# Kernel optimization log

Measured on AMD Instinct MI355X. Metric: run time of the kernel, lower is better.

The kernel has to match this reference:

```python
import jax, jax.numpy as jnp
import numpy as np

EMBED = 512
HEADS = 8
DH = EMBED // HEADS  # 64
M = 256              # num_landmarks
ITERS = 6            # pinv iterations
SCALE = DH ** -0.5
RES_K = 33           # lucidrains residual_conv_kernel default


def _layer_norm(x, g, b, eps=1e-5):
    mu = jnp.mean(x, axis=-1, keepdims=True)
    var = jnp.mean((x - mu) ** 2, axis=-1, keepdims=True)
    return (x - mu) / jnp.sqrt(var + eps) * g + b


def _pinv_iter(x, iters=ITERS):
    # Moore-Penrose iterative pseudo-inverse (lucidrains nystrom-attention)
    abs_x = jnp.abs(x)
    denom = jnp.max(abs_x.sum(-1)) * jnp.max(abs_x.sum(-2))
    z = jnp.swapaxes(x, -1, -2) / denom
    I = jnp.eye(x.shape[-1], dtype=x.dtype)
    for _ in range(iters):
        xz = x @ z
        z = 0.25 * z @ (13 * I - xz @ (15 * I - xz @ (7 * I - xz)))
    return z


def _dwconv2d(x, w, b):
    # x: [B,C,H,W], w: [C,1,kh,kw] depthwise, SAME padding (odd kernels == k//2)
    out = jax.lax.conv_general_dilated(x, w, (1, 1), 'SAME',
                                       dimension_numbers=('NCHW', 'OIHW', 'NCHW'),
                                       feature_group_count=x.shape[1])
    return out + b[None, :, None, None]


def _nystrom_attn(x, Wqkv, Wo, bo, res_w):
    # x: [B, n, EMBED]; pad at FRONT so n divisible by M (matches F.pad(..., padding, 0) semantics)
    b, n, _ = x.shape
    pad = (M - n % M) % M
    x = jnp.pad(x, ((0, 0), (pad, 0), (0, 0)))
    npad = n + pad
    qkv = x @ Wqkv.T                               # [b, npad, 3*EMBED]
    q, k, v = jnp.split(qkv, 3, axis=-1)
    to_heads = lambda t: t.reshape(b, npad, HEADS, DH).transpose(0, 2, 1, 3)  # bhnd
    q, k, v = to_heads(q), to_heads(k), to_heads(v)
    q = q * SCALE
    l = npad // M
    q_land = q.reshape(b, HEADS, M, l, DH).mean(3)  # [b,h,M,d]
    k_land = k.reshape(b, HEADS, M, l, DH).mean(3)
    s1 = jnp.einsum('bhnd,bhmd->bhnm', q, k_land)
    s2 = jnp.einsum('bhmd,bhld->bhml', q_land, k_land)
    s3 = jnp.einsum('bhmd,bhnd->bhmn', q_land, k)
    a1 = jax.nn.softmax(s1, -1)
    a2 = jax.nn.softmax(s2, -1)
    a3 = jax.nn.softmax(s3, -1)
    a2_inv = _pinv_iter(a2)
    out = a1 @ (a2_inv @ (a3 @ v))                 # [b,h,npad,d]
    # residual depthwise conv over v: channels=heads, spatial=(npad, DH), kernel (33,1)
    res = jax.lax.conv_general_dilated(v, res_w, (1, 1), 'SAME',
                                       dimension_numbers=('NCHW', 'OIHW', 'NCHW'),
                                       feature_group_count=HEADS)
    out = out + res
    out = out.transpose(0, 2, 1, 3).reshape(b, npad, EMBED)
    out = out @ Wo.T + bo
    return out[:, -n:]                             # drop front padding


def setup_inputs() -> dict:
    key = jax.random.key(0)
    ks = jax.random.split(key, 32)
    s = 0.02
    inp = {}
    inp['data'] = jax.random.normal(ks[0], (4, 4096, 1536), jnp.float32)
    inp['W1'] = jax.random.normal(ks[1], (EMBED, 1536), jnp.float32) * s
    inp['b1'] = jnp.zeros((EMBED,), jnp.float32)
    inp['cls_token'] = jax.random.normal(ks[2], (1, 1, EMBED), jnp.float32)
    for li, base in ((1, 3), (2, 9)):
        inp[f'ln{li}_g'] = jnp.ones((EMBED,), jnp.float32)
        inp[f'ln{li}_b'] = jnp.zeros((EMBED,), jnp.float32)
        inp[f'Wqkv{li}'] = jax.random.normal(ks[base], (3 * EMBED, EMBED), jnp.float32) * s
        inp[f'Wo{li}'] = jax.random.normal(ks[base + 1], (EMBED, EMBED), jnp.float32) * s
        inp[f'bo{li}'] = jnp.zeros((EMBED,), jnp.float32)
        inp[f'res{li}'] = jax.random.normal(ks[base + 2], (HEADS, 1, RES_K, 1), jnp.float32) * s
    inp['pw7'] = jax.random.normal(ks[15], (EMBED, 1, 7, 7), jnp.float32) * s
    inp['pb7'] = jnp.zeros((EMBED,), jnp.float32)
    inp['pw5'] = jax.random.normal(ks[16], (EMBED, 1, 5, 5), jnp.float32) * s
    inp['pb5'] = jnp.zeros((EMBED,), jnp.float32)
    inp['pw3'] = jax.random.normal(ks[17], (EMBED, 1, 3, 3), jnp.float32) * s
    inp['pb3'] = jnp.zeros((EMBED,), jnp.float32)
    inp['lnf_g'] = jnp.ones((EMBED,), jnp.float32)
    inp['lnf_b'] = jnp.zeros((EMBED,), jnp.float32)
    inp['W2'] = jax.random.normal(ks[18], (2, EMBED), jnp.float32) * s
    inp['b2'] = jnp.zeros((2,), jnp.float32)
    return inp


def reference(data, W1, b1, cls_token, ln1_g, ln1_b, Wqkv1, Wo1, bo1, res1,
              ln2_g, ln2_b, Wqkv2, Wo2, bo2, res2,
              pw7, pb7, pw5, pb5, pw3, pb3, lnf_g, lnf_b, W2, b2):
    h = jax.nn.relu(data @ W1.T + b1)              # [B, N, EMBED]
    B, N, C = h.shape
    grid = int(np.ceil(np.sqrt(N)))
    add = grid * grid - N
    if add > 0:
        h = jnp.concatenate([h, h[:, :add]], axis=1)
    cls = jnp.broadcast_to(cls_token, (B, 1, C))
    h = jnp.concatenate([cls, h], axis=1)          # [B, 1+grid^2, C]
    # TransLayer 1
    h = h + _nystrom_attn(_layer_norm(h, ln1_g, ln1_b), Wqkv1, Wo1, bo1, res1)
    # PPEG
    cls_t, feat = h[:, :1], h[:, 1:]
    cnn = feat.transpose(0, 2, 1).reshape(B, C, grid, grid)
    x = _dwconv2d(cnn, pw7, pb7) + cnn + _dwconv2d(cnn, pw5, pb5) + _dwconv2d(cnn, pw3, pb3)
    feat = x.reshape(B, C, grid * grid).transpose(0, 2, 1)
    h = jnp.concatenate([cls_t, feat], axis=1)
    # TransLayer 2
    h = h + _nystrom_attn(_layer_norm(h, ln2_g, ln2_b), Wqkv2, Wo2, bo2, res2)
    h = _layer_norm(h, lnf_g, lnf_b)
    cls_feat = h[:, 0]
    logits = cls_feat @ W2.T + b2
    Y_prob = jax.nn.softmax(logits, -1)
    Y_hat = jnp.argmax(Y_prob, -1)
    return logits, Y_prob, Y_hat
```

## Files before the change

### kernel.cpp

```cpp
#include <hip/hip_runtime.h>
#include <math.h>

#define EMBED 512
#define HEADS 8
#define DH 64
#define MM 256
#define LSEG 17
#define NPAD 4352
#define NTOK 4097
#define N0 4096
#define BATCH 4
#define CIN 1536
#define QSCALE 0.125f
#define BH 32
#define NSEG 17

typedef float fp32x4 __attribute__((ext_vector_type(4)));
typedef short bf16x8 __attribute__((ext_vector_type(8)));
typedef short bf16x4 __attribute__((ext_vector_type(4)));
typedef unsigned short u16;

__device__ __forceinline__ unsigned short f2bf(float f) {
  unsigned int u = __float_as_uint(f);
  u += 0x7fffu + ((u >> 16) & 1u);
  return (unsigned short)(u >> 16);
}
__device__ __forceinline__ float bf2f(unsigned short u) {
  return __uint_as_float((unsigned)u << 16);
}

__device__ __forceinline__ float block_sum(float v, float* red) {
  #pragma unroll
  for (int o = 1; o < 64; o <<= 1) v += __shfl_xor(v, o);
  int lane = threadIdx.x & 63, wid = threadIdx.x >> 6;
  if (lane == 0) red[wid] = v;
  __syncthreads();
  float r = red[0] + red[1] + red[2] + red[3];
  __syncthreads();
  return r;
}
__device__ __forceinline__ float block_max(float v, float* red) {
  #pragma unroll
  for (int o = 1; o < 64; o <<= 1) v = fmaxf(v, __shfl_xor(v, o));
  int lane = threadIdx.x & 63, wid = threadIdx.x >> 6;
  if (lane == 0) red[wid] = v;
  __syncthreads();
  float r = fmaxf(fmaxf(red[0], red[1]), fmaxf(red[2], red[3]));
  __syncthreads();
  return r;
}

__global__ void f2bf_kernel(const float* __restrict__ in, u16* __restrict__ out, int n) {
  int t = (blockIdx.x * 256 + threadIdx.x) * 8;
  if (t >= n) return;
  float4 a = *(const float4*)&in[t];
  float4 b = *(const float4*)&in[t + 4];
  bf16x8 pk;
  pk[0]=(short)f2bf(a.x); pk[1]=(short)f2bf(a.y); pk[2]=(short)f2bf(a.z); pk[3]=(short)f2bf(a.w);
  pk[4]=(short)f2bf(b.x); pk[5]=(short)f2bf(b.y); pk[6]=(short)f2bf(b.z); pk[7]=(short)f2bf(b.w);
  *(bf16x8*)&out[t] = pk;
}

__global__ __launch_bounds__(256) void gemm_abt(
    const u16* __restrict__ A, const u16* __restrict__ W,
    int Mrows, int Ncols, int K, const float* __restrict__ bias,
    float* __restrict__ fout, float* __restrict__ fout2,
    u16* __restrict__ uo0, u16* __restrict__ uo1, u16* __restrict__ uo2,
    int mode)
{
  __shared__ u16 As[64][40];
  __shared__ u16 Ws[128][40];
  int tid = threadIdx.x;
  int lane = tid & 63;
  int wv = tid >> 6;
  int rowBase = blockIdx.y * 64, colBase = blockIdx.x * 128;
  int quad = lane >> 4;
  int l15 = lane & 15;
  int sr = tid >> 2;
  int skc = (tid & 3) * 8;

  fp32x4 acc[8];
  #pragma unroll
  for (int i = 0; i < 8; i++) acc[i] = fp32x4{0,0,0,0};

  for (int kb = 0; kb < K; kb += 32) {
    __syncthreads();
    {
      int grow = rowBase + sr;
      bf16x8 av;
      if (grow < Mrows) av = *(const bf16x8*)&A[(size_t)grow * K + kb + skc];
      else { bf16x8 z = {0,0,0,0,0,0,0,0}; av = z; }
      *(bf16x8*)&As[sr][skc] = av;
    }
    #pragma unroll
    for (int h = 0; h < 2; h++) {
      int r = sr + h * 64;
      *(bf16x8*)&Ws[r][skc] =
          *(const bf16x8*)&W[(size_t)(colBase + r) * K + kb + skc];
    }
    __syncthreads();
    bf16x8 aF = *(const bf16x8*)&As[wv * 16 + l15][quad * 8];
    #pragma unroll
    for (int ct = 0; ct < 8; ct++) {
      bf16x8 bF = *(const bf16x8*)&Ws[ct * 16 + l15][quad * 8];
      acc[ct] = __builtin_amdgcn_mfma_f32_16x16x32_bf16(aF, bF, acc[ct], 0, 0, 0);
    }
  }

  #pragma unroll
  for (int ct = 0; ct < 8; ct++) {
    int col = colBase + ct * 16 + l15;
    #pragma unroll
    for (int i = 0; i < 4; i++) {
      int row = rowBase + wv * 16 + quad * 4 + i;
      if (row >= Mrows) continue;
      float v = acc[ct][i];
      if (mode == 0) {
        v += bias[col];
        v = fmaxf(v, 0.f);
        int b = row / N0, n = row % N0;
        fout[((size_t)b * NTOK + 1 + n) * EMBED + col] = v;
      } else if (mode == 1) {
        int b = row / NPAD, n = row % NPAD;
        int sec = col / EMBED;
        int hh = (col % EMBED) / DH;
        int d = col & 63;
        u16* dst = (sec == 0) ? uo0 : ((sec == 1) ? uo1 : uo2);
        if (sec == 0) v *= QSCALE;
        dst[(((size_t)b * HEADS + hh) * NPAD + n) * DH + d] = f2bf(v);
      } else if (mode == 2) {
        v += bias[col];
        fout[(size_t)row * EMBED + col] += v;
      } else {
        v += bias[col];
        float full = fout[(size_t)row * EMBED + col] + v;
        fout[(size_t)row * EMBED + col] = full;
        int b = row / NTOK, t = row % NTOK;
        if (t > 0) fout2[((size_t)b * N0 + (t - 1)) * EMBED + col] = full;
      }
    }
  }
}

__global__ __launch_bounds__(256) void gemm_nn2(
    const u16* __restrict__ A, const u16* __restrict__ Bc,
    u16* __restrict__ Cr, u16* __restrict__ Cc,
    int Nsize, float beta, float sgn, float gamma)
{
  __shared__ u16 As[64][40];
  __shared__ u16 Bs[64][40];
  int batch = blockIdx.z;
  const u16* Ab = A + (size_t)batch * MM * MM;
  const u16* Bb = Bc + (size_t)batch * MM * Nsize;
  int tid = threadIdx.x;
  int lane = tid & 63, wv = tid >> 6, quad = lane >> 4, l15 = lane & 15;
  int rowBase = blockIdx.y * 64, colBase = blockIdx.x * 64;
  int sr = tid >> 2, skc = (tid & 3) * 8;
  fp32x4 acc[4] = {fp32x4{0,0,0,0}, fp32x4{0,0,0,0}, fp32x4{0,0,0,0}, fp32x4{0,0,0,0}};

  for (int kb = 0; kb < MM; kb += 32) {
    __syncthreads();
    *(bf16x8*)&As[sr][skc] = *(const bf16x8*)&Ab[(size_t)(rowBase + sr) * MM + kb + skc];
    *(bf16x8*)&Bs[sr][skc] = *(const bf16x8*)&Bb[(size_t)(colBase + sr) * MM + kb + skc];
    __syncthreads();
    bf16x8 aF = *(const bf16x8*)&As[wv * 16 + l15][quad * 8];
    #pragma unroll
    for (int ct = 0; ct < 4; ct++) {
      bf16x8 bF = *(const bf16x8*)&Bs[ct * 16 + l15][quad * 8];
      acc[ct] = __builtin_amdgcn_mfma_f32_16x16x32_bf16(aF, bF, acc[ct], 0, 0, 0);
    }
  }

  #pragma unroll
  for (int ct = 0; ct < 4; ct++) {
    int col = colBase + ct * 16 + l15;
    #pragma unroll
    for (int i = 0; i < 4; i++) {
      int row = rowBase + wv * 16 + quad * 4 + i;
      float v = sgn * acc[ct][i];
      if (beta != 0.f) v += beta * bf2f(Ab[(size_t)row * MM + col]);
      v *= gamma;
      u16 o = f2bf(v);
      if (Cr) Cr[(size_t)batch * MM * Nsize + (size_t)row * Nsize + col] = o;
      if (Cc) Cc[(size_t)batch * MM * Nsize + (size_t)col * MM + row] = o;
    }
  }
}

__global__ void cls_kernel(const float* __restrict__ cls, float* __restrict__ h) {
  int t = blockIdx.x * blockDim.x + threadIdx.x;
  if (t >= BATCH * EMBED) return;
  int b = t / EMBED, c = t % EMBED;
  h[(size_t)b * NTOK * EMBED + c] = cls[c];
}

__global__ void zero_pad_kernel(u16* __restrict__ xpad) {
  int t = blockIdx.x * blockDim.x + threadIdx.x;
  const int per = 255 * EMBED;
  if (t >= BATCH * per) return;
  int b = t / per, r = t % per;
  xpad[(size_t)b * NPAD * EMBED + r] = 0;
}

__global__ __launch_bounds__(256) void ln_pad_kernel(
    const float* __restrict__ h, const float* __restrict__ g,
    const float* __restrict__ be, u16* __restrict__ xpad)
{
  __shared__ float red[4];
  int row = blockIdx.x;
  int b = row / NTOK, j = row % NTOK;
  const float* x = h + (size_t)row * EMBED;
  int tid = threadIdx.x;
  float v0 = x[tid], v1 = x[tid + 256];
  float mu = block_sum(v0 + v1, red) * (1.f / 512.f);
  float d0 = v0 - mu, d1 = v1 - mu;
  float var = block_sum(d0 * d0 + d1 * d1, red) * (1.f / 512.f);
  float inv = 1.f / sqrtf(var + 1e-5f);
  u16* o = xpad + ((size_t)b * NPAD + 255 + j) * EMBED;
  o[tid]       = f2bf(d0 * inv * g[tid]       + be[tid]);
  o[tid + 256] = f2bf(d1 * inv * g[tid + 256] + be[tid + 256]);
}

__global__ __launch_bounds__(256) void landmarks_kernel(
    const u16* __restrict__ q, const u16* __restrict__ k,
    float* __restrict__ qland, float* __restrict__ kland)
{
  int bh = blockIdx.y;
  int m = blockIdx.x * 4 + (threadIdx.x >> 6);
  int d = threadIdx.x & 63;
  const u16* qb = q + (size_t)bh * NPAD * DH;
  const u16* kb = k + (size_t)bh * NPAD * DH;
  float sq = 0.f, sk = 0.f;
  int base = m * LSEG;
  #pragma unroll
  for (int t = 0; t < LSEG; t++) {
    sq += bf2f(qb[(size_t)(base + t) * DH + d]);
    sk += bf2f(kb[(size_t)(base + t) * DH + d]);
  }
  qland[((size_t)bh * MM + m) * DH + d] = sq * (1.f / LSEG);
  kland[((size_t)bh * MM + m) * DH + d] = sk * (1.f / LSEG);
}

__global__ __launch_bounds__(256) void s2_softmax_kernel(
    const float* __restrict__ qland, const float* __restrict__ kland,
    u16* __restrict__ a2)
{
  __shared__ float qrow[64];
  __shared__ float red[4];
  int bh = blockIdx.y, m = blockIdx.x, tid = threadIdx.x;
  if (tid < 64) qrow[tid] = qland[((size_t)bh * MM + m) * DH + tid];
  __syncthreads();
  const float* kb = kland + (size_t)bh * MM * DH + (size_t)tid * DH;
  float s = 0.f;
  #pragma unroll 16
  for (int d = 0; d < 64; d++) s += qrow[d] * kb[d];
  float mx = block_max(s, red);
  float e = __expf(s - mx);
  float tot = block_sum(e, red);
  a2[((size_t)bh * MM + m) * MM + tid] = f2bf(e / tot);
}

__global__ void init_denom_kernel(float* __restrict__ denoms) {
  if (threadIdx.x < 2) denoms[threadIdx.x] = 0.f;
}

__global__ __launch_bounds__(256) void denom_kernel(
    const u16* __restrict__ a2, float* __restrict__ denoms)
{
  __shared__ float red[4];
  int bh = blockIdx.x, tid = threadIdx.x;
  const u16* A = a2 + (size_t)bh * MM * MM;
  float rs = 0.f, cs = 0.f;
  for (int j = 0; j < MM; j++) rs += bf2f(A[(size_t)tid * MM + j]);
  for (int i = 0; i < MM; i++) cs += bf2f(A[(size_t)i * MM + tid]);
  float mr = block_max(rs, red);
  float mc = block_max(cs, red);
  if (tid == 0) {
    atomicMax((int*)&denoms[0], __float_as_int(mr));
    atomicMax((int*)&denoms[1], __float_as_int(mc));
  }
}

__global__ __launch_bounds__(256) void z0_trans_kernel(
    const u16* __restrict__ a2, const float* __restrict__ denoms,
    u16* __restrict__ zr, u16* __restrict__ zc)
{
  __shared__ u16 tile[64][72];
  int bh = blockIdx.z, i0 = blockIdx.y * 64, j0 = blockIdx.x * 64;
  int tid = threadIdx.x;
  float inv = 1.f / (denoms[0] * denoms[1]);
  const u16* Ab = a2 + (size_t)bh * MM * MM;
  #pragma unroll
  for (int it = 0; it < 4; it++) {
    int idx = it * 1024 + tid * 4;
    int r = idx >> 6, c = idx & 63;
    bf16x4 v = *(const bf16x4*)&Ab[(size_t)(i0 + r) * MM + j0 + c];
    u16 o[4];
    #pragma unroll
    for (int j = 0; j < 4; j++) o[j] = f2bf(bf2f((unsigned short)v[j]) * inv);
    *(bf16x4*)&zc[(size_t)bh * MM * MM + (size_t)(i0 + r) * MM + j0 + c] = *(bf16x4*)o;
    #pragma unroll
    for (int j = 0; j < 4; j++) tile[c + j][r] = o[j];
  }
  __syncthreads();
  #pragma unroll
  for (int it = 0; it < 4; it++) {
    int idx = it * 1024 + tid * 4;
    int r = idx >> 6, c = idx & 63;
    u16 o[4] = {tile[r][c], tile[r][c + 1], tile[r][c + 2], tile[r][c + 3]};
    *(bf16x4*)&zr[(size_t)bh * MM * MM + (size_t)(j0 + r) * MM + i0 + c] = *(bf16x4*)o;
  }
}

__global__ __launch_bounds__(256) void a3v_part_mfma(
    const float* __restrict__ qland, const u16* __restrict__ k,
    const u16* __restrict__ v, u16* __restrict__ Opart,
    float* __restrict__ mpart, float* __restrict__ lpart)
{
  __shared__ __align__(16) u16 qs[64][40];
  __shared__ __align__(16) u16 ks[256][72];
  __shared__ __align__(16) u16 vt[64][72];
  int tid = threadIdx.x;
  int lane = tid & 63, wv = tid >> 6, quad = lane >> 4, l15 = lane & 15;
  int bh = blockIdx.y;
  int ltile = blockIdx.x & 3;
  int seg = blockIdx.x >> 2;
  int l0 = ltile * 64;
  int key0 = seg * 256;
  const float* qb = qland + (size_t)bh * MM * DH;
  const u16* kb = k + (size_t)bh * NPAD * DH;
  const u16* vb = v + (size_t)bh * NPAD * DH;

  {
    int sr = tid >> 2, dc = (tid & 3) * 16;
    const float4* p = (const float4*)&qb[(size_t)(l0 + sr) * DH + dc];
    float4 v0 = p[0], v1 = p[1], v2 = p[2], v3 = p[3];
    float va[16] = {v0.x,v0.y,v0.z,v0.w, v1.x,v1.y,v1.z,v1.w,
                    v2.x,v2.y,v2.z,v2.w, v3.x,v3.y,v3.z,v3.w};
    bf16x8 p0, p1;
    #pragma unroll
    for (int j = 0; j < 8; j++) { p0[j] = (short)f2bf(va[j]); p1[j] = (short)f2bf(va[8 + j]); }
    *(bf16x8*)&qs[sr][dc] = p0;
    *(bf16x8*)&qs[sr][dc + 8] = p1;
  }
  #pragma unroll
  for (int i = 0; i < 16; i++) {
    int idx = i * 1024 + tid * 4;
    int r = idx >> 6, c = idx & 63;
    *(bf16x4*)&ks[r][c] = *(const bf16x4*)&kb[(size_t)(key0 + r) * DH + c];
  }
  __syncthreads();

  fp32x4 sacc[16];
  #pragma unroll
  for (int ct = 0; ct < 16; ct++) sacc[ct] = fp32x4{0,0,0,0};
  bf16x8 aF0 = *(const bf16x8*)&qs[wv * 16 + l15][quad * 8];
  bf16x8 aF1 = *(const bf16x8*)&qs[wv * 16 + l15][32 + quad * 8];
  #pragma unroll
  for (int ct = 0; ct < 16; ct++) {
    bf16x8 b0 = *(const bf16x8*)&ks[ct * 16 + l15][quad * 8];
    bf16x8 b1 = *(const bf16x8*)&ks[ct * 16 + l15][32 + quad * 8];
    sacc[ct] = __builtin_amdgcn_mfma_f32_16x16x32_bf16(aF0, b0, sacc[ct], 0, 0, 0);
    sacc[ct] = __builtin_amdgcn_mfma_f32_16x16x32_bf16(aF1, b1, sacc[ct], 0, 0, 0);
  }

  float mrow[4], lrow[4];
  #pragma unroll
  for (int i = 0; i < 4; i++) {
    float m = -3.0e38f;
    #pragma unroll
    for (int ct = 0; ct < 16; ct++) m = fmaxf(m, sacc[ct][i]);
    #pragma unroll
    for (int o = 1; o < 16; o <<= 1) m = fmaxf(m, __shfl_xor(m, o));
    float s = 0.f;
    #pragma unroll
    for (int ct = 0; ct < 16; ct++) {
      float e = __expf(sacc[ct][i] - m);
      sacc[ct][i] = e;
      s += e;
    }
    #pragma unroll
    for (int o = 1; o < 16; o <<= 1) s += __shfl_xor(s, o);
    mrow[i] = m;
    lrow[i] = s;
  }
  __syncthreads();
  u16* P = &ks[0][0];
  #pragma unroll
  for (int ct = 0; ct < 16; ct++)
    #pragma unroll
    for (int i = 0; i < 4; i++)
      P[(size_t)(wv * 16 + quad * 4 + i) * 264 + ct * 16 + l15] = f2bf(sacc[ct][i]);
  __syncthreads();

  fp32x4 oacc[4] = {fp32x4{0,0,0,0}, fp32x4{0,0,0,0}, fp32x4{0,0,0,0}, fp32x4{0,0,0,0}};
  int dh = tid & 63, kgrp = tid >> 6;
  for (int ch = 0; ch < 4; ch++) {
    if (ch) __syncthreads();
    {
      int kbase = kgrp * 16;
      #pragma unroll
      for (int g = 0; g < 4; g++) {
        u16 pk[4];
        #pragma unroll
        for (int r = 0; r < 4; r++)
          pk[r] = vb[(size_t)(key0 + ch * 64 + kbase + g * 4 + r) * DH + dh];
        *(bf16x4*)&vt[dh][kbase + g * 4] = *(bf16x4*)pk;
      }
    }
    __syncthreads();
    #pragma unroll
    for (int ks2 = 0; ks2 < 2; ks2++) {
      bf16x8 aP = *(const bf16x8*)&P[(size_t)(wv * 16 + l15) * 264 + ch * 64 + ks2 * 32 + quad * 8];
      #pragma unroll
      for (int ct = 0; ct < 4; ct++) {
        bf16x8 bV = *(const bf16x8*)&vt[ct * 16 + l15][ks2 * 32 + quad * 8];
        oacc[ct] = __builtin_amdgcn_mfma_f32_16x16x32_bf16(aP, bV, oacc[ct], 0, 0, 0);
      }
    }
  }

  size_t base = ((size_t)seg * BH + bh) * MM + l0;
  #pragma unroll
  for (int ct = 0; ct < 4; ct++)
    #pragma unroll
    for (int i = 0; i < 4; i++) {
      int row = wv * 16 + quad * 4 + i;
      Opart[(base + row) * DH + ct * 16 + l15] = f2bf(oacc[ct][i]);
    }
  if (l15 == 0) {
    #pragma unroll
    for (int i = 0; i < 4; i++) {
      int row = wv * 16 + quad * 4 + i;
      mpart[base + row] = mrow[i];
      lpart[base + row] = lrow[i];
    }
  }
}

__global__ __launch_bounds__(256) void a3v_merge_kernel(
    const u16* __restrict__ Opart, const float* __restrict__ mpart,
    const float* __restrict__ lpart, u16* __restrict__ kvT)
{
  int bh = blockIdx.y;
  int lbase = blockIdx.x * 64;
  int d = threadIdx.x & 63, lsub = threadIdx.x >> 6;
  for (int li = lsub; li < 64; li += 4) {
    int lm = lbase + li;
    float M = -3.0e38f;
    #pragma unroll
    for (int s = 0; s < NSEG; s++)
      M = fmaxf(M, mpart[((size_t)s * BH + bh) * MM + lm]);
    float L = 0.f, O = 0.f;
    #pragma unroll
    for (int s = 0; s < NSEG; s++) {
      size_t idx = ((size_t)s * BH + bh) * MM + lm;
      float w = __expf(mpart[idx] - M);
      L += lpart[idx] * w;
      O += bf2f(Opart[idx * DH + d]) * w;
    }
    kvT[((size_t)bh * DH + d) * MM + lm] = f2bf(O / L);
  }
}

__global__ __launch_bounds__(256, 2) void attn1_mfma(
    const u16* __restrict__ q, const float* __restrict__ kland,
    const u16* __restrict__ kv2T, const u16* __restrict__ v,
    const float* __restrict__ resw, u16* __restrict__ attn)
{
  __shared__ __align__(16) u16 qs[64][40];
  __shared__ __align__(16) u16 klp[256][72];
  __shared__ __align__(16) u16 kvs[64][264];
  __shared__ float wsm[33];
  int tid = threadIdx.x;
  int lane = tid & 63, wv = tid >> 6, quad = lane >> 4, l15 = lane & 15;
  int bh = blockIdx.y, b = bh >> 3, hh = bh & 7;
  int n0 = 255 + blockIdx.x * 64;
  const u16* qb  = q + (size_t)bh * NPAD * DH;
  const float* klb = kland + (size_t)bh * MM * DH;
  const u16* kvb = kv2T + (size_t)bh * DH * MM;
  const u16* vb  = v + (size_t)bh * NPAD * DH;
  if (tid < 33) wsm[tid] = resw[hh * 33 + tid];

  {
    int sr = tid >> 2, dc = (tid & 3) * 16;
    int g = n0 + sr; if (g > NPAD - 1) g = NPAD - 1;
    *(bf16x8*)&qs[sr][dc]     = *(const bf16x8*)&qb[(size_t)g * DH + dc];
    *(bf16x8*)&qs[sr][dc + 8] = *(const bf16x8*)&qb[(size_t)g * DH + dc + 8];
  }
  #pragma unroll
  for (int i = 0; i < 16; i++) {
    int idx = i * 1024 + tid * 4;
    int r = idx >> 6, c = idx & 63;
    float4 vv = *(const float4*)&klb[(size_t)r * DH + c];
    bf16x4 pk = { (short)f2bf(vv.x), (short)f2bf(vv.y), (short)f2bf(vv.z), (short)f2bf(vv.w) };
    *(bf16x4*)&klp[r][c] = pk;
  }
  #pragma unroll
  for (int i = 0; i < 8; i++) {
    int idx = i * 2048 + tid * 8;
    int r = idx >> 8, c = idx & 255;
    *(bf16x8*)&kvs[r][c] = *(const bf16x8*)&kvb[(size_t)r * MM + c];
  }
  __syncthreads();

  fp32x4 sacc[16];
  #pragma unroll
  for (int ct = 0; ct < 16; ct++) sacc[ct] = fp32x4{0,0,0,0};
  bf16x8 aF0 = *(const bf16x8*)&qs[wv * 16 + l15][quad * 8];
  bf16x8 aF1 = *(const bf16x8*)&qs[wv * 16 + l15][32 + quad * 8];
  #pragma unroll
  for (int ct = 0; ct < 16; ct++) {
    bf16x8 b0 = *(const bf16x8*)&klp[ct * 16 + l15][quad * 8];
    bf16x8 b1 = *(const bf16x8*)&klp[ct * 16 + l15][32 + quad * 8];
    sacc[ct] = __builtin_amdgcn_mfma_f32_16x16x32_bf16(aF0, b0, sacc[ct], 0, 0, 0);
    sacc[ct] = __builtin_amdgcn_mfma_f32_16x16x32_bf16(aF1, b1, sacc[ct], 0, 0, 0);
  }
  #pragma unroll
  for (int i = 0; i < 4; i++) {
    float m = -3.0e38f;
    #pragma unroll
    for (int ct = 0; ct < 16; ct++) m = fmaxf(m, sacc[ct][i]);
    #pragma unroll
    for (int o = 1; o < 16; o <<= 1) m = fmaxf(m, __shfl_xor(m, o));
    float s = 0.f;
    #pragma unroll
    for (int ct = 0; ct < 16; ct++) {
      float e = __expf(sacc[ct][i] - m);
      sacc[ct][i] = e;
      s += e;
    }
    #pragma unroll
    for (int o = 1; o < 16; o <<= 1) s += __shfl_xor(s, o);
    float inv = 1.f / s;
    #pragma unroll
    for (int ct = 0; ct < 16; ct++) sacc[ct][i] *= inv;
  }
  __syncthreads();
  u16* P = &klp[0][0];
  #pragma unroll
  for (int ct = 0; ct < 16; ct++)
    #pragma unroll
    for (int i = 0; i < 4; i++)
      P[(size_t)(wv * 16 + quad * 4 + i) * 264 + ct * 16 + l15] = f2bf(sacc[ct][i]);
  __syncthreads();

  fp32x4 oacc[4] = {fp32x4{0,0,0,0}, fp32x4{0,0,0,0}, fp32x4{0,0,0,0}, fp32x4{0,0,0,0}};
  #pragma unroll
  for (int ks = 0; ks < 8; ks++) {
    bf16x8 aP = *(const bf16x8*)&P[(size_t)(wv * 16 + l15) * 264 + ks * 32 + quad * 8];
    #pragma unroll
    for (int ct = 0; ct < 4; ct++) {
      bf16x8 bV = *(const bf16x8*)&kvs[ct * 16 + l15][ks * 32 + quad * 8];
      oacc[ct] = __builtin_amdgcn_mfma_f32_16x16x32_bf16(aP, bV, oacc[ct], 0, 0, 0);
    }
  }
  __syncthreads();
  float* vwin = (float*)&kvs[0][0];
  #pragma unroll
  for (int i = 0; i < 6; i++) {
    int r = i * 16 + (tid >> 4), c = (tid & 15) * 4;
    int g = n0 - 16 + r;
    float4 vv;
    if (g <= NPAD - 1) {
      bf16x4 bv = *(const bf16x4*)&vb[(size_t)g * DH + c];
      vv.x = bf2f((unsigned short)bv[0]); vv.y = bf2f((unsigned short)bv[1]);
      vv.z = bf2f((unsigned short)bv[2]); vv.w = bf2f((unsigned short)bv[3]);
    } else { vv.x = 0.f; vv.y = 0.f; vv.z = 0.f; vv.w = 0.f; }
    *(float4*)&vwin[r * 68 + c] = vv;
  }
  __syncthreads();
  #pragma unroll
  for (int ct = 0; ct < 4; ct++) {
    int c = ct * 16 + l15;
    #pragma unroll
    for (int i = 0; i < 4; i++) {
      int rl = wv * 16 + quad * 4 + i;
      int n = n0 + rl;
      if (n > NPAD - 1) continue;
      float ca = 0.f;
      #pragma unroll 11
      for (int t = 0; t < 33; t++) ca += vwin[(rl + t) * 68 + c] * wsm[t];
      attn[((size_t)b * NTOK + (n - 255)) * EMBED + hh * DH + c] = f2bf(oacc[ct][i] + ca);
    }
  }
}

__global__ void prep_wcomb_kernel(
    const float* __restrict__ pw7, const float* __restrict__ pw5,
    const float* __restrict__ pw3, const float* __restrict__ pb7,
    const float* __restrict__ pb5, const float* __restrict__ pb3,
    float* __restrict__ wcomb, float* __restrict__ biasc)
{
  int i = blockIdx.x * blockDim.x + threadIdx.x;
  if (i < EMBED * 49) {
    int c = i / 49, tap = i % 49;
    int ky = tap / 7, kx = tap % 7;
    float v = pw7[c * 49 + tap];
    if (ky >= 1 && ky <= 5 && kx >= 1 && kx <= 5) v += pw5[c * 25 + (ky - 1) * 5 + (kx - 1)];
    if (ky >= 2 && ky <= 4 && kx >= 2 && kx <= 4) v += pw3[c * 9 + (ky - 2) * 3 + (kx - 2)];
    if (ky == 3 && kx == 3) v += 1.f;
    wcomb[tap * EMBED + c] = v;
  }
  if (i < EMBED) biasc[i] = pb7[i] + pb5[i] + pb3[i];
}

__global__ __launch_bounds__(256) void dwconv_kernel(
    const float* __restrict__ tmp, const float* __restrict__ wcomb,
    const float* __restrict__ biasc, float* __restrict__ h)
{
  __shared__ float4 wsm[49][32];
  int tx = threadIdx.x;
  int ty = threadIdx.y;
  int cb = blockIdx.x * 128;
  int c = cb + tx * 4;
  int b = blockIdx.z;
  int n = blockIdx.y * 8 + ty;
  int y = n >> 6, x = n & 63;
  int tid = ty * 32 + tx;
  for (int i = tid; i < 49 * 32; i += 256) {
    int tap = i >> 5, g = i & 31;
    wsm[tap][g] = *(const float4*)&wcomb[tap * EMBED + cb + g * 4];
  }
  __syncthreads();
  const float* src = tmp + (size_t)b * N0 * EMBED;
  float4 acc = *(const float4*)&biasc[c];
  #pragma unroll
  for (int ky = 0; ky < 7; ky++) {
    int yy = y + ky - 3;
    if (yy < 0 || yy >= 64) continue;
    #pragma unroll
    for (int kx = 0; kx < 7; kx++) {
      int xx = x + kx - 3;
      if (xx < 0 || xx >= 64) continue;
      float4 vv = *(const float4*)&src[((size_t)yy * 64 + xx) * EMBED + c];
      float4 w = wsm[ky * 7 + kx][tx];
      acc.x += vv.x * w.x;
      acc.y += vv.y * w.y;
      acc.z += vv.z * w.z;
      acc.w += vv.w * w.w;
    }
  }
  *(float4*)&h[((size_t)b * NTOK + 1 + n) * EMBED + c] = acc;
}

__global__ __launch_bounds__(256) void final_kernel(
    const float* __restrict__ h, const float* __restrict__ g,
    const float* __restrict__ be, const float* __restrict__ W2,
    const float* __restrict__ b2, float* __restrict__ out)
{
  __shared__ float red[4];
  int b = blockIdx.x, tid = threadIdx.x;
  const float* x = h + (size_t)b * NTOK * EMBED;
  float v0 = x[tid], v1 = x[tid + 256];
  float mu = block_sum(v0 + v1, red) * (1.f / 512.f);
  float d0 = v0 - mu, d1 = v1 - mu;
  float var = block_sum(d0 * d0 + d1 * d1, red) * (1.f / 512.f);
  float inv = 1.f / sqrtf(var + 1e-5f);
  float xn0 = d0 * inv * g[tid] + be[tid];
  float xn1 = d1 * inv * g[tid + 256] + be[tid + 256];
  float l0 = block_sum(xn0 * W2[tid] + xn1 * W2[tid + 256], red);
  float l1 = block_sum(xn0 * W2[512 + tid] + xn1 * W2[512 + tid + 256], red);
  if (tid == 0) {
    l0 += b2[0]; l1 += b2[1];
    out[b * 2 + 0] = l0;
    out[b * 2 + 1] = l1;
    float mx = fmaxf(l0, l1);
    float e0 = expf(l0 - mx), e1 = expf(l1 - mx);
    float s = e0 + e1;
    out[8 + b * 2 + 0] = e0 / s;
    out[8 + b * 2 + 1] = e1 / s;
    out[16 + b] = (l1 > l0) ? 1.f : 0.f;
  }
}

extern "C" void kernel_launch(void* const* d_in, const int* in_sizes, int n_in,
                              void* d_out, int out_size, void* d_ws, size_t ws_size,
                              hipStream_t stream)
{
  const float* data = (const float*)d_in[0];
  const float* W1   = (const float*)d_in[1];
  const float* b1   = (const float*)d_in[2];
  const float* cls  = (const float*)d_in[3];
  const float* lng[2]  = {(const float*)d_in[4],  (const float*)d_in[10]};
  const float* lnb[2]  = {(const float*)d_in[5],  (const float*)d_in[11]};
  const float* Wqkv[2] = {(const float*)d_in[6],  (const float*)d_in[12]};
  const float* Wo[2]   = {(const float*)d_in[7],  (const float*)d_in[13]};
  const float* bo[2]   = {(const float*)d_in[8],  (const float*)d_in[14]};
  const float* resw[2] = {(const float*)d_in[9],  (const float*)d_in[15]};
  const float* pw7 = (const float*)d_in[16];
  const float* pb7 = (const float*)d_in[17];
  const float* pw5 = (const float*)d_in[18];
  const float* pb5 = (const float*)d_in[19];
  const float* pw3 = (const float*)d_in[20];
  const float* pb3 = (const float*)d_in[21];
  const float* lnfg = (const float*)d_in[22];
  const float* lnfb = (const float*)d_in[23];
  const float* W2  = (const float*)d_in[24];
  const float* b2  = (const float*)d_in[25];

  float* ws = (float*)d_ws;
  size_t off = 0;
  auto alloc = [&](size_t n) { float* p = ws + off; off += n; return p; };
  float* hbuf   = alloc((size_t)BATCH * NTOK * EMBED);
  float* xpadf  = alloc((size_t)BATCH * NPAD * EMBED);
  float* qbuff  = alloc((size_t)BH * NPAD * DH);
  float* kbuff  = alloc((size_t)BH * NPAD * DH);
  float* vbuff  = alloc((size_t)BH * NPAD * DH);
  float* qland  = alloc((size_t)BH * MM * DH);
  float* kland  = alloc((size_t)BH * MM * DH);
  float* a2f    = alloc((size_t)BH * MM * MM / 2);
  float* zaRf   = alloc((size_t)BH * MM * MM / 2);
  float* zaCf   = alloc((size_t)BH * MM * MM / 2);
  float* zbRf   = alloc((size_t)BH * MM * MM / 2);
  float* zbCf   = alloc((size_t)BH * MM * MM / 2);
  float* xzRf   = alloc((size_t)BH * MM * MM / 2);
  float* xzCf   = alloc((size_t)BH * MM * MM / 2);
  float* t1Cf   = alloc((size_t)BH * MM * MM / 2);
  float* t2Cf   = alloc((size_t)BH * MM * MM / 2);
  float* kvTf   = alloc((size_t)BH * MM * DH / 2);
  float* kv2Tf  = alloc((size_t)BH * MM * DH / 2);
  float* wqkvbf = alloc((size_t)2 * 3 * EMBED * EMBED / 2);
  float* wobf   = alloc((size_t)2 * EMBED * EMBED / 2);
  float* wcomb  = alloc(49 * EMBED);
  float* biasc  = alloc(EMBED);
  float* denoms = alloc(64);
  float* mpart  = alloc((size_t)NSEG * BH * MM);
  float* lpart  = alloc((size_t)NSEG * BH * MM);

  u16* xpadB = (u16*)xpadf;
  u16* qB = (u16*)qbuff;
  u16* kB = (u16*)kbuff;
  u16* vB = (u16*)vbuff;
  u16* a2B = (u16*)a2f;
  u16* zaR = (u16*)zaRf; u16* zaC = (u16*)zaCf;
  u16* zbR = (u16*)zbRf; u16* zbC = (u16*)zbCf;
  u16* xzR = (u16*)xzRf; u16* xzC = (u16*)xzCf;
  u16* t1C = (u16*)t1Cf; u16* t2C = (u16*)t2Cf;
  u16* kvT = (u16*)kvTf; u16* kv2T = (u16*)kv2Tf;
  u16* attnB = xpadB;
  u16* OpartB = zaR;
  u16* databf = (u16*)qbuff;
  u16* W1bf = (u16*)vbuff;
  u16* WqkvB[2] = {(u16*)wqkvbf, (u16*)wqkvbf + (size_t)3 * EMBED * EMBED};
  u16* WoB[2]   = {(u16*)wobf,   (u16*)wobf + (size_t)EMBED * EMBED};
  float* convtmp = qbuff;

  int ndata = BATCH * N0 * CIN;
  f2bf_kernel<<<dim3((ndata / 8 + 255) / 256), 256, 0, stream>>>(data, databf, ndata);
  f2bf_kernel<<<dim3((EMBED * CIN / 8 + 255) / 256), 256, 0, stream>>>(W1, W1bf, EMBED * CIN);
  for (int l = 0; l < 2; l++) {
    f2bf_kernel<<<dim3((3 * EMBED * EMBED / 8 + 255) / 256), 256, 0, stream>>>(Wqkv[l], WqkvB[l], 3 * EMBED * EMBED);
    f2bf_kernel<<<dim3((EMBED * EMBED / 8 + 255) / 256), 256, 0, stream>>>(Wo[l], WoB[l], EMBED * EMBED);
  }

  gemm_abt<<<dim3(EMBED / 128, (BATCH * N0) / 64), 256, 0, stream>>>(
      databf, W1bf, BATCH * N0, EMBED, CIN, b1, hbuf, nullptr, nullptr, nullptr, nullptr, 0);
  cls_kernel<<<dim3((BATCH * EMBED + 255) / 256), 256, 0, stream>>>(cls, hbuf);

  for (int layer = 0; layer < 2; layer++) {
    ln_pad_kernel<<<dim3(BATCH * NTOK), 256, 0, stream>>>(hbuf, lng[layer], lnb[layer], xpadB);
    zero_pad_kernel<<<dim3((BATCH * 255 * EMBED + 255) / 256), 256, 0, stream>>>(xpadB);
    gemm_abt<<<dim3((3 * EMBED) / 128, (BATCH * NPAD) / 64), 256, 0, stream>>>(
        xpadB, WqkvB[layer], BATCH * NPAD, 3 * EMBED, EMBED, nullptr,
        nullptr, nullptr, qB, kB, vB, 1);
    landmarks_kernel<<<dim3(MM / 4, BH), 256, 0, stream>>>(qB, kB, qland, kland);
    s2_softmax_kernel<<<dim3(MM, BH), 256, 0, stream>>>(qland, kland, a2B);
    init_denom_kernel<<<1, 64, 0, stream>>>(denoms);
    denom_kernel<<<dim3(BH), 256, 0, stream>>>(a2B, denoms);

    a3v_part_mfma<<<dim3(4 * NSEG, BH), 256, 0, stream>>>(
        qland, kB, vB, OpartB, mpart, lpart);
    a3v_merge_kernel<<<dim3(MM / 64, BH), 256, 0, stream>>>(OpartB, mpart, lpart, kvT);

    z0_trans_kernel<<<dim3(4, 4, BH), 256, 0, stream>>>(a2B, denoms, zaR, zaC);
    u16 *zinR = zaR, *zinC = zaC, *zoutR = zbR, *zoutC = zbC;
    for (int it = 0; it < 6; it++) {
      gemm_nn2<<<dim3(4, 4, BH), 256, 0, stream>>>(a2B, zinC, xzR, xzC, MM, 0.f, 1.f, 1.f);
      gemm_nn2<<<dim3(4, 4, BH), 256, 0, stream>>>(xzR, xzC, nullptr, t1C, MM, 7.f, -1.f, 1.f);
      gemm_nn2<<<dim3(4, 4, BH), 256, 0, stream>>>(xzR, t1C, nullptr, t2C, MM, 15.f, -1.f, 1.f);
      gemm_nn2<<<dim3(4, 4, BH), 256, 0, stream>>>(zinR, t2C, zoutR, zoutC, MM, 13.f, -1.f, 0.25f);
      u16* t;
      t = zinR; zinR = zoutR; zoutR = t;
      t = zinC; zinC = zoutC; zoutC = t;
    }
    gemm_nn2<<<dim3(1, 4, BH), 256, 0, stream>>>(zinR, kvT, nullptr, kv2T, DH, 0.f, 1.f, 1.f);
    attn1_mfma<<<dim3((NTOK + 63) / 64, BH), 256, 0, stream>>>(
        qB, kland, kv2T, vB, resw[layer], attnB);
    gemm_abt<<<dim3(EMBED / 128, (BATCH * NTOK + 63) / 64), 256, 0, stream>>>(
        attnB, WoB[layer], BATCH * NTOK, EMBED, EMBED, bo[layer], hbuf,
        (layer == 0) ? convtmp : nullptr, nullptr, nullptr, nullptr,
        (layer == 0) ? 3 : 2);

    if (layer == 0) {
      prep_wcomb_kernel<<<dim3((EMBED * 49 + 255) / 256), 256, 0, stream>>>(
          pw7, pw5, pw3, pb7, pb5, pb3, wcomb, biasc);
      dwconv_kernel<<<dim3(EMBED / 128, N0 / 8, BATCH), dim3(32, 8), 0, stream>>>(
          convtmp, wcomb, biasc, hbuf);
    }
  }

  final_kernel<<<dim3(BATCH), 256, 0, stream>>>(hbuf, lnfg, lnfb, W2, b2, (float*)d_out);
}
```

Before: 1.589 ms.

## Compute residual conv via Toeplitz MFMA and read operands directly from global

The 33-tap residual depthwise convolution is rewritten as a bf16 Toeplitz matrix product on MFMA, using a per-head 64x96 band matrix prebuilt once by a new kernel. The scalar fp32 LDS loop it replaces goes away. The landmarks kernel now also writes bf16 key landmarks, so attn1 loads K-landmarks, Q and kv2T fragments straight from global memory instead of staging them in LDS. LDS usage drops to one buffer and the launch bound rises to 4 blocks per SM to raise occupancy. In exchange the conv weights and V window are rounded to bf16, and global reads are repeated across waves.

```diff
diff --git a/kernel.cpp b/kernel.cpp
--- a/kernel.cpp
+++ b/kernel.cpp
@@ -223,7 +223,7 @@
 
 __global__ __launch_bounds__(256) void landmarks_kernel(
     const u16* __restrict__ q, const u16* __restrict__ k,
-    float* __restrict__ qland, float* __restrict__ kland)
+    float* __restrict__ qland, float* __restrict__ kland, u16* __restrict__ klandB)
 {
   int bh = blockIdx.y;
   int m = blockIdx.x * 4 + (threadIdx.x >> 6);
@@ -237,8 +237,10 @@
     sq += bf2f(qb[(size_t)(base + t) * DH + d]);
     sk += bf2f(kb[(size_t)(base + t) * DH + d]);
   }
+  float kv = sk * (1.f / LSEG);
   qland[((size_t)bh * MM + m) * DH + d] = sq * (1.f / LSEG);
-  kland[((size_t)bh * MM + m) * DH + d] = sk * (1.f / LSEG);
+  kland[((size_t)bh * MM + m) * DH + d] = kv;
+  klandB[((size_t)bh * MM + m) * DH + d] = f2bf(kv);
 }
 
 __global__ __launch_bounds__(256) void s2_softmax_kernel(
@@ -463,56 +465,45 @@
   }
 }
 
-__global__ __launch_bounds__(256, 2) void attn1_mfma(
-    const u16* __restrict__ q, const float* __restrict__ kland,
+__global__ void prep_toep_kernel(const float* __restrict__ resw0,
+                                 const float* __restrict__ resw1,
+                                 u16* __restrict__ toepB)
+{
+  int i = blockIdx.x * 256 + threadIdx.x;
+  if (i >= 2 * 8 * 64 * 96) return;
+  int t = i % 96, r = (i / 96) % 64, hh = (i / (96 * 64)) % 8, l = i / (96 * 64 * 8);
+  const float* rw = l ? resw1 : resw0;
+  int tap = t - r;
+  float v = (tap >= 0 && tap <= 32) ? rw[hh * 33 + tap] : 0.f;
+  toepB[i] = f2bf(v);
+}
+
+__global__ __launch_bounds__(256, 4) void attn1_mfma(
+    const u16* __restrict__ q, const u16* __restrict__ klandB,
     const u16* __restrict__ kv2T, const u16* __restrict__ v,
-    const float* __restrict__ resw, u16* __restrict__ attn)
-{
-  __shared__ __align__(16) u16 qs[64][40];
-  __shared__ __align__(16) u16 klp[256][72];
-  __shared__ __align__(16) u16 kvs[64][264];
-  __shared__ float wsm[33];
+    const u16* __restrict__ toep, u16* __restrict__ attn)
+{
+  __shared__ __align__(16) u16 buf[64 * 264];
   int tid = threadIdx.x;
   int lane = tid & 63, wv = tid >> 6, quad = lane >> 4, l15 = lane & 15;
   int bh = blockIdx.y, b = bh >> 3, hh = bh & 7;
   int n0 = 255 + blockIdx.x * 64;
   const u16* qb  = q + (size_t)bh * NPAD * DH;
-  const float* klb = kland + (size_t)bh * MM * DH;
+  const u16* klb = klandB + (size_t)bh * MM * DH;
   const u16* kvb = kv2T + (size_t)bh * DH * MM;
   const u16* vb  = v + (size_t)bh * NPAD * DH;
-  if (tid < 33) wsm[tid] = resw[hh * 33 + tid];
-
-  {
-    int sr = tid >> 2, dc = (tid & 3) * 16;
-    int g = n0 + sr; if (g > NPAD - 1) g = NPAD - 1;
-    *(bf16x8*)&qs[sr][dc]     = *(const bf16x8*)&qb[(size_t)g * DH + dc];
-    *(bf16x8*)&qs[sr][dc + 8] = *(const bf16x8*)&qb[(size_t)g * DH + dc + 8];
-  }
-  #pragma unroll
-  for (int i = 0; i < 16; i++) {
-    int idx = i * 1024 + tid * 4;
-    int r = idx >> 6, c = idx & 63;
-    float4 vv = *(const float4*)&klb[(size_t)r * DH + c];
-    bf16x4 pk = { (short)f2bf(vv.x), (short)f2bf(vv.y), (short)f2bf(vv.z), (short)f2bf(vv.w) };
-    *(bf16x4*)&klp[r][c] = pk;
-  }
-  #pragma unroll
-  for (int i = 0; i < 8; i++) {
-    int idx = i * 2048 + tid * 8;
-    int r = idx >> 8, c = idx & 255;
-    *(bf16x8*)&kvs[r][c] = *(const bf16x8*)&kvb[(size_t)r * MM + c];
-  }
-  __syncthreads();
-
+  const u16* tb  = toep + (size_t)hh * 64 * 96;
+
+  int qrow = n0 + wv * 16 + l15; if (qrow > NPAD - 1) qrow = NPAD - 1;
+  bf16x8 aF0 = *(const bf16x8*)&qb[(size_t)qrow * DH + quad * 8];
+  bf16x8 aF1 = *(const bf16x8*)&qb[(size_t)qrow * DH + 32 + quad * 8];
   fp32x4 sacc[16];
   #pragma unroll
   for (int ct = 0; ct < 16; ct++) sacc[ct] = fp32x4{0,0,0,0};
-  bf16x8 aF0 = *(const bf16x8*)&qs[wv * 16 + l15][quad * 8];
-  bf16x8 aF1 = *(const bf16x8*)&qs[wv * 16 + l15][32 + quad * 8];
   #pragma unroll
   for (int ct = 0; ct < 16; ct++) {
-    bf16x8 b0 = *(const bf16x8*)&klp[ct * 16 + l15][quad * 8];
-    bf16x8 b1 = *(const bf16x8*)&klp[ct * 16 + l15][32 + quad * 8];
+    bf16x8 b0 = *(const bf16x8*)&klb[(size_t)(ct * 16 + l15) * DH + quad * 8];
+    bf16x8 b1 = *(const bf16x8*)&klb[(size_t)(ct * 16 + l15) * DH + 32 + quad * 8];
     sacc[ct] = __builtin_amdgcn_mfma_f32_16x16x32_bf16(aF0, b0, sacc[ct], 0, 0, 0);
     sacc[ct] = __builtin_amdgcn_mfma_f32_16x16x32_bf16(aF1, b1, sacc[ct], 0, 0, 0);
   }
@@ -536,40 +527,51 @@
     #pragma unroll
     for (int ct = 0; ct < 16; ct++) sacc[ct][i] *= inv;
   }
-  __syncthreads();
-  u16* P = &klp[0][0];
   #pragma unroll
   for (int ct = 0; ct < 16; ct++)
     #pragma unroll
     for (int i = 0; i < 4; i++)
-      P[(size_t)(wv * 16 + quad * 4 + i) * 264 + ct * 16 + l15] = f2bf(sacc[ct][i]);
+      buf[(size_t)(wv * 16 + quad * 4 + i) * 264 + ct * 16 + l15] = f2bf(sacc[ct][i]);
   __syncthreads();
 
   fp32x4 oacc[4] = {fp32x4{0,0,0,0}, fp32x4{0,0,0,0}, fp32x4{0,0,0,0}, fp32x4{0,0,0,0}};
   #pragma unroll
   for (int ks = 0; ks < 8; ks++) {
-    bf16x8 aP = *(const bf16x8*)&P[(size_t)(wv * 16 + l15) * 264 + ks * 32 + quad * 8];
+    bf16x8 aP = *(const bf16x8*)&buf[(size_t)(wv * 16 + l15) * 264 + ks * 32 + quad * 8];
     #pragma unroll
     for (int ct = 0; ct < 4; ct++) {
-      bf16x8 bV = *(const bf16x8*)&kvs[ct * 16 + l15][ks * 32 + quad * 8];
+      bf16x8 bV = *(const bf16x8*)&kvb[(size_t)(ct * 16 + l15) * MM + ks * 32 + quad * 8];
       oacc[ct] = __builtin_amdgcn_mfma_f32_16x16x32_bf16(aP, bV, oacc[ct], 0, 0, 0);
     }
   }
   __syncthreads();
-  float* vwin = (float*)&kvs[0][0];
-  #pragma unroll
-  for (int i = 0; i < 6; i++) {
-    int r = i * 16 + (tid >> 4), c = (tid & 15) * 4;
-    int g = n0 - 16 + r;
-    float4 vv;
-    if (g <= NPAD - 1) {
-      bf16x4 bv = *(const bf16x4*)&vb[(size_t)g * DH + c];
-      vv.x = bf2f((unsigned short)bv[0]); vv.y = bf2f((unsigned short)bv[1]);
-      vv.z = bf2f((unsigned short)bv[2]); vv.w = bf2f((unsigned short)bv[3]);
-    } else { vv.x = 0.f; vv.y = 0.f; vv.z = 0.f; vv.w = 0.f; }
-    *(float4*)&vwin[r * 68 + c] = vv;
-  }
-  __syncthreads();
+
+  {
+    int d = lane;
+    #pragma unroll
+    for (int tt4 = 0; tt4 < 6; tt4++) {
+      u16 vals[4];
+      #pragma unroll
+      for (int j = 0; j < 4; j++) {
+        int t = wv * 24 + tt4 * 4 + j;
+        int g = n0 - 16 + t;
+        vals[j] = (g <= NPAD - 1) ? vb[(size_t)g * DH + d] : (u16)0;
+      }
+      *(bf16x4*)&buf[d * 104 + wv * 24 + tt4 * 4] = *(bf16x4*)vals;
+    }
+  }
+  __syncthreads();
+
+  #pragma unroll
+  for (int kc = 0; kc < 3; kc++) {
+    bf16x8 aT = *(const bf16x8*)&tb[(size_t)(wv * 16 + l15) * 96 + kc * 32 + quad * 8];
+    #pragma unroll
+    for (int ct = 0; ct < 4; ct++) {
+      bf16x8 bW = *(const bf16x8*)&buf[(ct * 16 + l15) * 104 + kc * 32 + quad * 8];
+      oacc[ct] = __builtin_amdgcn_mfma_f32_16x16x32_bf16(aT, bW, oacc[ct], 0, 0, 0);
+    }
+  }
+
   #pragma unroll
   for (int ct = 0; ct < 4; ct++) {
     int c = ct * 16 + l15;
@@ -578,10 +580,7 @@
       int rl = wv * 16 + quad * 4 + i;
       int n = n0 + rl;
       if (n > NPAD - 1) continue;
-      float ca = 0.f;
-      #pragma unroll 11
-      for (int t = 0; t < 33; t++) ca += vwin[(rl + t) * 68 + c] * wsm[t];
-      attn[((size_t)b * NTOK + (n - 255)) * EMBED + hh * DH + c] = f2bf(oacc[ct][i] + ca);
+      attn[((size_t)b * NTOK + (n - 255)) * EMBED + hh * DH + c] = f2bf(oacc[ct][i]);
     }
   }
 }
@@ -709,6 +708,7 @@
   float* vbuff  = alloc((size_t)BH * NPAD * DH);
   float* qland  = alloc((size_t)BH * MM * DH);
   float* kland  = alloc((size_t)BH * MM * DH);
+  float* klandBf= alloc((size_t)BH * MM * DH / 2);
   float* a2f    = alloc((size_t)BH * MM * MM / 2);
   float* zaRf   = alloc((size_t)BH * MM * MM / 2);
   float* zaCf   = alloc((size_t)BH * MM * MM / 2);
@@ -722,6 +722,7 @@
   float* kv2Tf  = alloc((size_t)BH * MM * DH / 2);
   float* wqkvbf = alloc((size_t)2 * 3 * EMBED * EMBED / 2);
   float* wobf   = alloc((size_t)2 * EMBED * EMBED / 2);
+  float* toepf  = alloc((size_t)2 * 8 * 64 * 96 / 2);
   float* wcomb  = alloc(49 * EMBED);
   float* biasc  = alloc(EMBED);
   float* denoms = alloc(64);
@@ -732,6 +733,7 @@
   u16* qB = (u16*)qbuff;
   u16* kB = (u16*)kbuff;
   u16* vB = (u16*)vbuff;
+  u16* klandB = (u16*)klandBf;
   u16* a2B = (u16*)a2f;
   u16* zaR = (u16*)zaRf; u16* zaC = (u16*)zaCf;
   u16* zbR = (u16*)zbRf; u16* zbC = (u16*)zbCf;
@@ -744,6 +746,7 @@
   u16* W1bf = (u16*)vbuff;
   u16* WqkvB[2] = {(u16*)wqkvbf, (u16*)wqkvbf + (size_t)3 * EMBED * EMBED};
   u16* WoB[2]   = {(u16*)wobf,   (u16*)wobf + (size_t)EMBED * EMBED};
+  u16* toepB[2] = {(u16*)toepf,  (u16*)toepf + (size_t)8 * 64 * 96};
   float* convtmp = qbuff;
 
   int ndata = BATCH * N0 * CIN;
@@ -753,6 +756,8 @@
     f2bf_kernel<<<dim3((3 * EMBED * EMBED / 8 + 255) / 256), 256, 0, stream>>>(Wqkv[l], WqkvB[l], 3 * EMBED * EMBED);
     f2bf_kernel<<<dim3((EMBED * EMBED / 8 + 255) / 256), 256, 0, stream>>>(Wo[l], WoB[l], EMBED * EMBED);
   }
+  prep_toep_kernel<<<dim3((2 * 8 * 64 * 96 + 255) / 256), 256, 0, stream>>>(
+      resw[0], resw[1], (u16*)toepf);
 
   gemm_abt<<<dim3(EMBED / 128, (BATCH * N0) / 64), 256, 0, stream>>>(
       databf, W1bf, BATCH * N0, EMBED, CIN, b1, hbuf, nullptr, nullptr, nullptr, nullptr, 0);
@@ -764,7 +769,7 @@
     gemm_abt<<<dim3((3 * EMBED) / 128, (BATCH * NPAD) / 64), 256, 0, stream>>>(
         xpadB, WqkvB[layer], BATCH * NPAD, 3 * EMBED, EMBED, nullptr,
         nullptr, nullptr, qB, kB, vB, 1);
-    landmarks_kernel<<<dim3(MM / 4, BH), 256, 0, stream>>>(qB, kB, qland, kland);
+    landmarks_kernel<<<dim3(MM / 4, BH), 256, 0, stream>>>(qB, kB, qland, kland, klandB);
     s2_softmax_kernel<<<dim3(MM, BH), 256, 0, stream>>>(qland, kland, a2B);
     init_denom_kernel<<<1, 64, 0, stream>>>(denoms);
     denom_kernel<<<dim3(BH), 256, 0, stream>>>(a2B, denoms);
@@ -786,7 +791,7 @@
     }
     gemm_nn2<<<dim3(1, 4, BH), 256, 0, stream>>>(zinR, kvT, nullptr, kv2T, DH, 0.f, 1.f, 1.f);
     attn1_mfma<<<dim3((NTOK + 63) / 64, BH), 256, 0, stream>>>(
-        qB, kland, kv2T, vB, resw[layer], attnB);
+        qB, klandB, kv2T, vB, toepB[layer], attnB);
     gemm_abt<<<dim3(EMBED / 128, (BATCH * NTOK + 63) / 64), 256, 0, stream>>>(
         attnB, WoB[layer], BATCH * NTOK, EMBED, EMBED, bo[layer], hbuf,
         (layer == 0) ? convtmp : nullptr, nullptr, nullptr, nullptr,
```

Result: no change. 1.617 ms (+1.8%).
